# Kernel optimization log

Measured on AMD Instinct MI355X. Metric: run time of the kernel, lower is better.

Reference implementation:

```python
import jax, jax.numpy as jnp
import numpy as np

DIM = 2048
N_EXPERTS = 16
TOP_K = 4
MOE_INTER = 1024
SHARED_INTER = 2 * MOE_INTER  # n_shared_experts * moe_inter_dim
B, S = 4, 1024
INIT = 0.02


def setup_inputs() -> dict:
    key = jax.random.key(0)
    ks = jax.random.split(key, 8)
    return {
        "x": jax.random.normal(ks[0], (B, S, DIM), dtype=jnp.float32),
        "gate_w": jax.random.normal(ks[1], (DIM, N_EXPERTS), dtype=jnp.float32) * INIT,
        "w1": jax.random.normal(ks[2], (N_EXPERTS, DIM, MOE_INTER), dtype=jnp.float32) * INIT,
        "w2": jax.random.normal(ks[3], (N_EXPERTS, MOE_INTER, DIM), dtype=jnp.float32) * INIT,
        "w3": jax.random.normal(ks[4], (N_EXPERTS, DIM, MOE_INTER), dtype=jnp.float32) * INIT,
        "ws1": jax.random.normal(ks[5], (DIM, SHARED_INTER), dtype=jnp.float32) * INIT,
        "ws2": jax.random.normal(ks[6], (SHARED_INTER, DIM), dtype=jnp.float32) * INIT,
        "ws3": jax.random.normal(ks[7], (DIM, SHARED_INTER), dtype=jnp.float32) * INIT,
    }


def _moe_forward(x, gate_w, w1, w2, w3, ws1, ws2, ws3):
    shape = x.shape
    xf = x.reshape(-1, DIM)  # [T, D]
    # Gate: softmax scores, top-k selection (weights are the top-k probs)
    scores = jax.nn.softmax(xf @ gate_w, axis=-1)          # [T, E]
    weights, indices = jax.lax.top_k(scores, TOP_K)         # [T, K] each
    y = jnp.zeros_like(xf)
    # Fixed loop over experts (structural, not over data dims).
    for e in range(N_EXPERTS):
        # gate coefficient for expert e: 0 if not in token's top-k
        coef = jnp.sum(weights * (indices == e), axis=-1)   # [T]
        h = jax.nn.silu(xf @ w1[e]) * (xf @ w3[e])          # [T, I]
        y = y + coef[:, None] * (h @ w2[e])
    # Shared experts (always-on gated MLP)
    z = (jax.nn.silu(xf @ ws1) * (xf @ ws3)) @ ws2
    return (y + z).reshape(shape)


def reference(x, gate_w, w1, w2, w3, ws1, ws2, ws3):
    return _moe_forward(x, gate_w, w1, w2, w3, ws1, ws2, ws3)
```

## Files before the change

kernel.cpp:

```cpp
#include <hip/hip_runtime.h>
#include <hip/hip_bf16.h>
#include <stdint.h>

#define T_TOK 4096
#define DIMD  2048
#define NEXP  16
#define TOPK  4
#define NI    1024
#define NSH   2048

typedef __attribute__((ext_vector_type(8))) short short8;
typedef __attribute__((ext_vector_type(4))) float f32x4;
typedef __attribute__((ext_vector_type(4))) unsigned short u16x4;

__device__ __forceinline__ unsigned short f2bf(float f) {
    union { float f; unsigned u; } v; v.f = f;
    return (unsigned short)((v.u + 0x7fffu + ((v.u >> 16) & 1u)) >> 16);
}

__device__ __forceinline__ void gload16(const void* g, void* l) {
    __builtin_amdgcn_global_load_lds(
        (const __attribute__((address_space(1))) void*)g,
        (__attribute__((address_space(3))) void*)l, 16, 0, 0);
}

__global__ __launch_bounds__(256) void gwt_kernel(const float* __restrict__ gw,
                                                  float* __restrict__ gwT) {
    int i = blockIdx.x * 256 + threadIdx.x;
    int d = i >> 4, e = i & 15;
    gwT[e * DIMD + d] = gw[i];
}

__global__ __launch_bounds__(256) void gate_kernel(const float* __restrict__ x,
                                                   const float* __restrict__ gwT,
                                                   int* __restrict__ blk_cnt,
                                                   int* __restrict__ tk_er,
                                                   float* __restrict__ tk_wv) {
    __shared__ int h[16];
    const int blk = blockIdx.x;
    const int t = blk * 4 + (threadIdx.x >> 6);
    const int lane = threadIdx.x & 63;
    if (threadIdx.x < 16) h[threadIdx.x] = 0;
    __syncthreads();

    const f32x4* xr = (const f32x4*)(x + (size_t)t * DIMD);
    f32x4 xv[8];
#pragma unroll
    for (int i = 0; i < 8; ++i) xv[i] = xr[i * 64 + lane];

    float acc[NEXP];
#pragma unroll
    for (int e = 0; e < NEXP; ++e) {
        const f32x4* gr = (const f32x4*)(gwT + e * DIMD);
        float s = 0.f;
#pragma unroll
        for (int i = 0; i < 8; ++i) {
            f32x4 gv = gr[i * 64 + lane];
            s += xv[i][0] * gv[0] + xv[i][1] * gv[1] +
                 xv[i][2] * gv[2] + xv[i][3] * gv[3];
        }
        acc[e] = s;
    }
#pragma unroll
    for (int e = 0; e < NEXP; ++e) {
        float v = acc[e];
#pragma unroll
        for (int off = 32; off; off >>= 1) v += __shfl_xor(v, off, 64);
        acc[e] = v;
    }
    float m = acc[0];
#pragma unroll
    for (int e = 1; e < NEXP; ++e) m = fmaxf(m, acc[e]);
    float s = 0.f;
#pragma unroll
    for (int e = 0; e < NEXP; ++e) { acc[e] = expf(acc[e] - m); s += acc[e]; }
    float inv = 1.f / s;
#pragma unroll
    for (int e = 0; e < NEXP; ++e) acc[e] *= inv;

    float w4[TOPK]; int i4[TOPK];
#pragma unroll
    for (int k = 0; k < TOPK; ++k) {
        float bv = -1.f; int be = 0;
#pragma unroll
        for (int e = 0; e < NEXP; ++e)
            if (acc[e] > bv) { bv = acc[e]; be = e; }
        w4[k] = bv; i4[k] = be;
#pragma unroll
        for (int e = 0; e < NEXP; ++e)
            if (e == be) acc[e] = -1.f;
    }

    if (lane == 0) {
        int r4[TOPK];
#pragma unroll
        for (int k = 0; k < TOPK; ++k) r4[k] = atomicAdd(&h[i4[k]], 1);
#pragma unroll
        for (int k = 0; k < TOPK; ++k) {
            tk_er[t * 4 + k] = (i4[k] << 20) | r4[k];
            tk_wv[t * 4 + k] = w4[k];
        }
    }
    __syncthreads();
    if (threadIdx.x < 16) blk_cnt[blk * 16 + threadIdx.x] = h[threadIdx.x];
}

__global__ __launch_bounds__(256) void scan_kernel(const int* __restrict__ blk_cnt,
                                                   int* __restrict__ blk_off,
                                                   int* __restrict__ cnt,
                                                   int* __restrict__ offs,
                                                   int* __restrict__ table) {
    __shared__ int gsum[16][17];
    __shared__ int gbase[16][17];
    __shared__ int csh[16];
    int tid = threadIdx.x;
    int e = tid >> 4, g = tid & 15;
    {
        int s = 0;
        for (int b = g * 64; b < g * 64 + 64; ++b) s += blk_cnt[b * 16 + e];
        gsum[e][g] = s;
    }
    __syncthreads();
    if (tid < 16) {
        int run = 0;
        for (int g2 = 0; g2 < 16; ++g2) { gbase[tid][g2] = run; run += gsum[tid][g2]; }
        csh[tid] = run;
        cnt[tid] = run;
    }
    __syncthreads();
    {
        int run = gbase[e][g];
        for (int b = g * 64; b < g * 64 + 64; ++b) {
            blk_off[b * 16 + e] = run;
            run += blk_cnt[b * 16 + e];
        }
    }
    if (tid == 0) {
        int o = 0;
        for (int e2 = 0; e2 < 16; ++e2) { offs[e2] = o; o += csh[e2]; }
        offs[NEXP] = o;
        int ns = 0;
        for (int e2 = 0; e2 < 16; ++e2)
            for (int rb = 0; rb < csh[e2]; rb += 256) {
                table[ns] = e2; table[128 + ns] = rb; ++ns;
            }
        table[255] = ns;
    }
}

__global__ __launch_bounds__(256) void fill_kernel(const int* __restrict__ tk_er,
                                                   const float* __restrict__ tk_wv,
                                                   const int* __restrict__ blk_off,
                                                   int* __restrict__ list,
                                                   float* __restrict__ cw) {
    int i = blockIdx.x * 256 + threadIdx.x;
    int rec = tk_er[i];
    int e = rec >> 20, r = rec & 0xFFFFF;
    int t = i >> 2;
    int ro = blk_off[(t >> 2) * 16 + e] + r;
    list[e * T_TOK + ro] = t;
    cw[e * T_TOK + ro] = tk_wv[i];
}

__global__ __launch_bounds__(256) void cvt_kernel(const float* __restrict__ x,
                                                  unsigned short* __restrict__ xb) {
    int i = blockIdx.x * 256 + threadIdx.x;
    const f32x4* src = (const f32x4*)x;
    f32x4 a = src[i * 2 + 0];
    f32x4 b = src[i * 2 + 1];
    short8 o;
#pragma unroll
    for (int j = 0; j < 4; ++j) o[j] = (short)f2bf(a[j]);
#pragma unroll
    for (int j = 0; j < 4; ++j) o[4 + j] = (short)f2bf(b[j]);
    ((short8*)xb)[i] = o;
}

template <int MODE>
__global__ __launch_bounds__(256) void tq_kernel(const float* __restrict__ src,
                                                 unsigned short* __restrict__ dst,
                                                 int K, int N, size_t dstStrideE) {
    int e = blockIdx.z;
    src += (size_t)e * K * N;
    dst += (size_t)e * dstStrideE;
    __shared__ unsigned short tile[32][36];
    int t = threadIdx.x;
    int k0 = blockIdx.y * 32, n0 = blockIdx.x * 32;
    {
        int row = t >> 3, c4 = (t & 7) * 4;
        f32x4 v = *(const f32x4*)(src + (size_t)(k0 + row) * N + n0 + c4);
#pragma unroll
        for (int j = 0; j < 4; ++j) tile[row][c4 + j] = f2bf(v[j]);
    }
    __syncthreads();
    {
        int nn = t >> 3, kc = (t & 7) * 4;
        int n = n0 + nn;
        int r = (MODE == 0) ? n : ((n >> 4) * 32 + (MODE == 2 ? 16 : 0) + (n & 15));
        u16x4 o;
#pragma unroll
        for (int j = 0; j < 4; ++j) o[j] = tile[kc + j][nn];
        *(u16x4*)(dst + (size_t)r * K + k0 + kc) = o;
    }
}


#define STA4(base, kt) do { \
    gload16(gA[0][0] + (kt) * 64, (void*)(smem + (base) + ldsA[0][0])); \
    gload16(gA[0][1] + (kt) * 64, (void*)(smem + (base) + ldsA[0][1])); \
    gload16(gA[1][0] + (kt) * 64, (void*)(smem + (base) + ldsA[1][0])); \
    gload16(gA[1][1] + (kt) * 64, (void*)(smem + (base) + ldsA[1][1])); \
  } while (0)
#define STBU(base, kt, u) do { \
    gload16(gB[u][0] + (kt) * 64, (void*)(smem + (base) + ldsB[u][0])); \
    gload16(gB[u][1] + (kt) * 64, (void*)(smem + (base) + ldsB[u][1])); \
  } while (0)

#define RDA(base, MH) do { \
    _Pragma("unroll") \
    for (int m2 = 0; m2 < 4; ++m2) { \
      const char* bp = smem + (base) + (wm * 128 + (MH) * 64 + m2 * 16 + fr) * 128; \
      aF[m2][0] = *(const short8*)(bp + kA0); \
      aF[m2][1] = *(const short8*)(bp + kA1); \
    } } while (0)
#define RDB(dst, base, NH) do { \
    _Pragma("unroll") \
    for (int n2 = 0; n2 < 2; ++n2) { \
      const char* bp = smem + (base) + (wn * 64 + (NH) * 32 + n2 * 16 + fr) * 128; \
      dst[n2][0] = *(const short8*)(bp + kA0); \
      dst[n2][1] = *(const short8*)(bp + kA1); \
    } } while (0)

#define MM(MH, NH, BF) do { \
    __builtin_amdgcn_s_setprio(1); \
    _Pragma("unroll") \
    for (int m2 = 0; m2 < 4; ++m2) { \
      _Pragma("unroll") \
      for (int n2 = 0; n2 < 2; ++n2) { \
        acc[(MH) * 4 + m2][(NH) * 2 + n2] = __builtin_amdgcn_mfma_f32_16x16x32_bf16( \
            aF[m2][0], BF[n2][0], acc[(MH) * 4 + m2][(NH) * 2 + n2], 0, 0, 0); \
        acc[(MH) * 4 + m2][(NH) * 2 + n2] = __builtin_amdgcn_mfma_f32_16x16x32_bf16( \
            aF[m2][1], BF[n2][1], acc[(MH) * 4 + m2][(NH) * 2 + n2], 0, 0, 0); \
      } \
    } \
    __builtin_amdgcn_s_setprio(0); \
  } while (0)

template <int KIND>
__global__ __launch_bounds__(512, 2) void gemm8p(
    const unsigned short* __restrict__ A, const unsigned short* __restrict__ Ball,
    const int* __restrict__ cnt, const int* __restrict__ offs,
    const int* __restrict__ list, const float* __restrict__ cw,
    unsigned short* __restrict__ hout, float* __restrict__ fout,
    const int* __restrict__ table) {
    constexpr bool ROUTED = (KIND == 1 || KIND == 3);
    constexpr bool UP = (KIND <= 1);
    constexpr int K = (KIND <= 1) ? 2048 : 1024;
    constexpr int NT = K / 64;
    constexpr int ASTR = (KIND == 3) ? 1024 : 2048;
    constexpr int BSTR = (KIND == 3) ? 1024 : 2048;

    int bx, rb, e, M, obase;
    if constexpr (ROUTED) {
        int bid = blockIdx.x;
        int slot = bid >> 3;
        if (slot >= table[255]) return;
        bx = bid & 7;
        e = table[slot];
        rb = table[128 + slot];
        M = cnt[e];
        obase = offs[e];
    } else {
        bx = blockIdx.x; rb = blockIdx.y * 256; e = 0; M = T_TOK; obase = 0;
    }
    const int kb = (KIND == 2) ? blockIdx.z * 1024 : 0;
    const unsigned short* Bp = Ball +
        (KIND == 1 ? (size_t)e * 2048 * 2048 : KIND == 3 ? (size_t)e * 2048 * 1024 : 0);

    extern __shared__ char smem[];

    const int tid = threadIdx.x;
    const int lane = tid & 63, wid = tid >> 6;
    const int wm = wid >> 2, wn = wid & 3;
    const int fr = lane & 15, fq = lane >> 4;
    const int swz = (fr & 7) << 4;
    const int kA0 = (fq * 16) ^ swz;
    const int kA1 = (64 + fq * 16) ^ swz;

    int ldsA[2][2], ldsB[2][2];
    const unsigned short* gA[2][2];
    const unsigned short* gB[2][2];
#pragma unroll
    for (int u = 0; u < 2; ++u)
#pragma unroll
        for (int i = 0; i < 2; ++i) {
            int rowA = i * 128 + u * 64 + (tid >> 3);
            int kcA = (tid & 7) ^ (rowA & 7);
            ldsA[u][i] = i * 16384 + u * 8192 + tid * 16;
            int gr = rb + rowA;
            int cr = (gr < M) ? gr : (M - 1);
            size_t arow;
            if (KIND == 1)      arow = (size_t)list[e * T_TOK + cr];
            else if (KIND == 3) arow = (size_t)(obase + cr);
            else                arow = (size_t)gr;
            gA[u][i] = A + arow * ASTR + kb + kcA * 8;

            int s = (tid >> 8) + 2 * i;
            int rowB = s * 64 + u * 32 + ((tid >> 3) & 31);
            int kcB = (tid & 7) ^ (rowB & 7);
            ldsB[u][i] = s * 8192 + u * 4096 + (tid & 255) * 16;
            gB[u][i] = Bp + (size_t)(bx * 256 + rowB) * BSTR + kb + kcB * 8;
        }

    f32x4 acc[8][4];
#pragma unroll
    for (int m = 0; m < 8; ++m)
#pragma unroll
        for (int n = 0; n < 4; ++n) acc[m][n] = (f32x4)0.f;

    short8 aF[4][2], bF0[2][2], bF1[2][2];

    STBU(65536, 0, 0); STBU(65536, 0, 1);
    STBU(65536 + 32768, 1, 0); STBU(65536 + 32768, 1, 1);
    STA4(0, 0);
    asm volatile("s_waitcnt vmcnt(0)" ::: "memory");
    __builtin_amdgcn_s_barrier();

    int bB = 0, bB2 = 2;
    for (int t = 0; t < NT; ++t) {
        const int baseA = (t & 1) * 32768;
        const int baseAn = ((t + 1) & 1) * 32768;
        const int baseB = 65536 + bB * 32768;
        const int baseBn = 65536 + bB2 * 32768;
        const bool moreA = (t + 1 < NT);
        const bool moreB = (t + 2 < NT);

        RDA(baseA, 0); RDB(bF0, baseB, 0);
        if (moreA) STA4(baseAn, t + 1);
        if (moreB) { STBU(baseBn, t + 2, 0); STBU(baseBn, t + 2, 1); }
        MM(0, 0, bF0);
        RDB(bF1, baseB, 1);
        MM(0, 1, bF1);
        RDA(baseA, 1);
        MM(1, 1, bF1);
        MM(1, 0, bF0);
        if (moreB) { asm volatile("s_waitcnt vmcnt(4)" ::: "memory"); }
        else       { asm volatile("s_waitcnt vmcnt(0)" ::: "memory"); }
        __builtin_amdgcn_s_barrier();
        bB = (bB == 2) ? 0 : bB + 1;
        bB2 = (bB2 == 2) ? 0 : bB2 + 1;
    }

    if constexpr (UP) {
        constexpr int LDO = (KIND == 1) ? NI : NSH;
#pragma unroll
        for (int mf = 0; mf < 8; ++mf)
#pragma unroll
            for (int q = 0; q < 4; ++q) {
                int gr = rb + wm * 128 + mf * 16 + fq * 4 + q;
                if (gr < M) {
                    float coef = 1.f;
                    if constexpr (KIND == 1) coef = cw[e * T_TOK + gr];
                    size_t orow = (size_t)(obase + gr) * LDO;
#pragma unroll
                    for (int nfp = 0; nfp < 2; ++nfp) {
                        float c1 = acc[mf][2 * nfp][q], c3 = acc[mf][2 * nfp + 1][q];
                        float h = c1 / (1.f + __expf(-c1)) * c3 * coef;
                        int ncol = (bx * 8 + wn * 2 + nfp) * 16 + fr;
                        hout[orow + ncol] = f2bf(h);
                    }
                }
            }
    } else {
#pragma unroll
        for (int mf = 0; mf < 8; ++mf)
#pragma unroll
            for (int q = 0; q < 4; ++q) {
                int gr = rb + wm * 128 + mf * 16 + fq * 4 + q;
                if (gr < M) {
                    int orow = (KIND == 3) ? list[e * T_TOK + gr] : gr;
#pragma unroll
                    for (int nf = 0; nf < 4; ++nf) {
                        int col = bx * 256 + wn * 64 + nf * 16 + fr;
                        atomicAdd(fout + (size_t)orow * DIMD + col, acc[mf][nf][q]);
                    }
                }
            }
    }
}

extern "C" void kernel_launch(void* const* d_in, const int* in_sizes, int n_in,
                              void* d_out, int out_size, void* d_ws, size_t ws_size,
                              hipStream_t stream) {
    const float* x   = (const float*)d_in[0];
    const float* gw  = (const float*)d_in[1];
    const float* w1  = (const float*)d_in[2];
    const float* w2  = (const float*)d_in[3];
    const float* w3  = (const float*)d_in[4];
    const float* ws1 = (const float*)d_in[5];
    const float* ws2 = (const float*)d_in[6];
    const float* ws3 = (const float*)d_in[7];
    float* out = (float*)d_out;

    char* p = (char*)d_ws;
    unsigned short* xb   = (unsigned short*)p; p += (size_t)T_TOK * DIMD * 2;
    unsigned short* hs   = (unsigned short*)p; p += (size_t)T_TOK * NSH * 2;
    unsigned short* hbuf = (unsigned short*)p; p += (size_t)T_TOK * TOPK * NI * 2;
    unsigned short* upT  = (unsigned short*)p; p += (size_t)NEXP * 2048 * DIMD * 2;
    unsigned short* w2T  = (unsigned short*)p; p += (size_t)NEXP * DIMD * NI * 2;
    unsigned short* upsT = (unsigned short*)p; p += (size_t)2 * NSH * DIMD * 2;
    unsigned short* ws2T = (unsigned short*)p; p += (size_t)DIMD * NSH * 2;
    float* gwT = (float*)p;                    p += (size_t)NEXP * DIMD * 4;
    float* cw = (float*)p;                     p += (size_t)NEXP * T_TOK * 4;
    int* list = (int*)p;                       p += (size_t)NEXP * T_TOK * 4;
    int* tk_er = (int*)p;                      p += (size_t)T_TOK * TOPK * 4;
    float* tk_wv = (float*)p;                  p += (size_t)T_TOK * TOPK * 4;
    int* blk_cnt = (int*)p;                    p += (size_t)1024 * 16 * 4;
    int* blk_off = (int*)p;                    p += (size_t)1024 * 16 * 4;
    int* cnt = (int*)p;                        p += 256;
    int* offs = (int*)p;                       p += 256;
    int* table = (int*)p;                      p += 1024;
    if ((size_t)(p - (char*)d_ws) > ws_size) return;

    hipFuncSetAttribute((const void*)&gemm8p<0>, hipFuncAttributeMaxDynamicSharedMemorySize, 163840);
    hipFuncSetAttribute((const void*)&gemm8p<1>, hipFuncAttributeMaxDynamicSharedMemorySize, 163840);
    hipFuncSetAttribute((const void*)&gemm8p<2>, hipFuncAttributeMaxDynamicSharedMemorySize, 163840);
    hipFuncSetAttribute((const void*)&gemm8p<3>, hipFuncAttributeMaxDynamicSharedMemorySize, 163840);

    hipMemsetAsync(out, 0, (size_t)out_size * 4, stream);
    gwt_kernel<<<(NEXP * DIMD) / 256, 256, 0, stream>>>(gw, gwT);
    gate_kernel<<<T_TOK / 4, 256, 0, stream>>>(x, gwT, blk_cnt, tk_er, tk_wv);
    scan_kernel<<<1, 256, 0, stream>>>(blk_cnt, blk_off, cnt, offs, table);
    fill_kernel<<<T_TOK * TOPK / 256, 256, 0, stream>>>(tk_er, tk_wv, blk_off, list, cw);
    cvt_kernel<<<(T_TOK * DIMD / 8) / 256, 256, 0, stream>>>(x, xb);

    tq_kernel<1><<<dim3(NI / 32, DIMD / 32, NEXP), 256, 0, stream>>>(w1, upT, DIMD, NI, (size_t)2048 * DIMD);
    tq_kernel<2><<<dim3(NI / 32, DIMD / 32, NEXP), 256, 0, stream>>>(w3, upT, DIMD, NI, (size_t)2048 * DIMD);
    tq_kernel<1><<<dim3(NSH / 32, DIMD / 32, 1), 256, 0, stream>>>(ws1, upsT, DIMD, NSH, 0);
    tq_kernel<2><<<dim3(NSH / 32, DIMD / 32, 1), 256, 0, stream>>>(ws3, upsT, DIMD, NSH, 0);
    tq_kernel<0><<<dim3(DIMD / 32, NI / 32, NEXP), 256, 0, stream>>>(w2, w2T, NI, DIMD, (size_t)DIMD * NI);
    tq_kernel<0><<<dim3(DIMD / 32, NSH / 32, 1), 256, 0, stream>>>(ws2, ws2T, NSH, DIMD, 0);

    gemm8p<0><<<dim3(16, 16, 1), 512, 163840, stream>>>(
        xb, upsT, nullptr, nullptr, nullptr, nullptr, hs, nullptr, nullptr);
    gemm8p<2><<<dim3(8, 16, 2), 512, 163840, stream>>>(
        hs, ws2T, nullptr, nullptr, nullptr, nullptr, nullptr, out, nullptr);
    gemm8p<1><<<640, 512, 163840, stream>>>(
        xb, upT, cnt, offs, list, cw, hbuf, nullptr, table);
    gemm8p<3><<<640, 512, 163840, stream>>>(
        hbuf, w2T, cnt, offs, list, nullptr, nullptr, out, table);
}
```

Measured before the change: 715.4 us.

## Shrink GEMM tiles to 128x256 with BK=32 triple-buffered pipeline for higher occupancy

Reworks the bf16 MFMA GEMM from 256x256 tiles with BK=64 and a large LDS footprint to 128x256 tiles with BK=32 and a 3-stage ring buffer in 72KB of LDS. Launch bounds rise to 4 blocks per CU, the grids and the routed slot table double (the table now packs expert and row base into one int), and a new swizzled LDS read layout is added. The aim is more concurrent waves and less padding waste on the routed experts. The cost is lower reuse per tile, more global loads per FLOP, and more atomic and barrier overhead.

```diff
diff --git a/kernel.cpp b/kernel.cpp
--- a/kernel.cpp
+++ b/kernel.cpp
@@ -141,8 +141,8 @@
         offs[NEXP] = o;
         int ns = 0;
         for (int e2 = 0; e2 < 16; ++e2)
-            for (int rb = 0; rb < csh[e2]; rb += 256) {
-                table[ns] = e2; table[128 + ns] = rb; ++ns;
+            for (int rb = 0; rb < csh[e2]; rb += 128) {
+                table[ns] = (e2 << 16) | rb; ++ns;
             }
         table[255] = ns;
     }
@@ -204,50 +204,8 @@
     }
 }
 
-
-#define STA4(base, kt) do { \
-    gload16(gA[0][0] + (kt) * 64, (void*)(smem + (base) + ldsA[0][0])); \
-    gload16(gA[0][1] + (kt) * 64, (void*)(smem + (base) + ldsA[0][1])); \
-    gload16(gA[1][0] + (kt) * 64, (void*)(smem + (base) + ldsA[1][0])); \
-    gload16(gA[1][1] + (kt) * 64, (void*)(smem + (base) + ldsA[1][1])); \
-  } while (0)
-#define STBU(base, kt, u) do { \
-    gload16(gB[u][0] + (kt) * 64, (void*)(smem + (base) + ldsB[u][0])); \
-    gload16(gB[u][1] + (kt) * 64, (void*)(smem + (base) + ldsB[u][1])); \
-  } while (0)
-
-#define RDA(base, MH) do { \
-    _Pragma("unroll") \
-    for (int m2 = 0; m2 < 4; ++m2) { \
-      const char* bp = smem + (base) + (wm * 128 + (MH) * 64 + m2 * 16 + fr) * 128; \
-      aF[m2][0] = *(const short8*)(bp + kA0); \
-      aF[m2][1] = *(const short8*)(bp + kA1); \
-    } } while (0)
-#define RDB(dst, base, NH) do { \
-    _Pragma("unroll") \
-    for (int n2 = 0; n2 < 2; ++n2) { \
-      const char* bp = smem + (base) + (wn * 64 + (NH) * 32 + n2 * 16 + fr) * 128; \
-      dst[n2][0] = *(const short8*)(bp + kA0); \
-      dst[n2][1] = *(const short8*)(bp + kA1); \
-    } } while (0)
-
-#define MM(MH, NH, BF) do { \
-    __builtin_amdgcn_s_setprio(1); \
-    _Pragma("unroll") \
-    for (int m2 = 0; m2 < 4; ++m2) { \
-      _Pragma("unroll") \
-      for (int n2 = 0; n2 < 2; ++n2) { \
-        acc[(MH) * 4 + m2][(NH) * 2 + n2] = __builtin_amdgcn_mfma_f32_16x16x32_bf16( \
-            aF[m2][0], BF[n2][0], acc[(MH) * 4 + m2][(NH) * 2 + n2], 0, 0, 0); \
-        acc[(MH) * 4 + m2][(NH) * 2 + n2] = __builtin_amdgcn_mfma_f32_16x16x32_bf16( \
-            aF[m2][1], BF[n2][1], acc[(MH) * 4 + m2][(NH) * 2 + n2], 0, 0, 0); \
-      } \
-    } \
-    __builtin_amdgcn_s_setprio(0); \
-  } while (0)
-
 template <int KIND>
-__global__ __launch_bounds__(512, 2) void gemm8p(
+__global__ __launch_bounds__(512, 4) void gemm8p(
     const unsigned short* __restrict__ A, const unsigned short* __restrict__ Ball,
     const int* __restrict__ cnt, const int* __restrict__ offs,
     const int* __restrict__ list, const float* __restrict__ cw,
@@ -256,7 +214,7 @@
     constexpr bool ROUTED = (KIND == 1 || KIND == 3);
     constexpr bool UP = (KIND <= 1);
     constexpr int K = (KIND <= 1) ? 2048 : 1024;
-    constexpr int NT = K / 64;
+    constexpr int NT = K / 32;
     constexpr int ASTR = (KIND == 3) ? 1024 : 2048;
     constexpr int BSTR = (KIND == 3) ? 1024 : 2048;
 
@@ -266,12 +224,13 @@
         int slot = bid >> 3;
         if (slot >= table[255]) return;
         bx = bid & 7;
-        e = table[slot];
-        rb = table[128 + slot];
+        int pk = table[slot];
+        e = pk >> 16;
+        rb = pk & 0xFFFF;
         M = cnt[e];
         obase = offs[e];
     } else {
-        bx = blockIdx.x; rb = blockIdx.y * 256; e = 0; M = T_TOK; obase = 0;
+        bx = blockIdx.x; rb = blockIdx.y * 128; e = 0; M = T_TOK; obase = 0;
     }
     const int kb = (KIND == 2) ? blockIdx.z * 1024 : 0;
     const unsigned short* Bp = Ball +
@@ -283,88 +242,94 @@
     const int lane = tid & 63, wid = tid >> 6;
     const int wm = wid >> 2, wn = wid & 3;
     const int fr = lane & 15, fq = lane >> 4;
-    const int swz = (fr & 7) << 4;
-    const int kA0 = (fq * 16) ^ swz;
-    const int kA1 = (64 + fq * 16) ^ swz;
-
-    int ldsA[2][2], ldsB[2][2];
-    const unsigned short* gA[2][2];
-    const unsigned short* gB[2][2];
-#pragma unroll
-    for (int u = 0; u < 2; ++u)
-#pragma unroll
-        for (int i = 0; i < 2; ++i) {
-            int rowA = i * 128 + u * 64 + (tid >> 3);
-            int kcA = (tid & 7) ^ (rowA & 7);
-            ldsA[u][i] = i * 16384 + u * 8192 + tid * 16;
-            int gr = rb + rowA;
-            int cr = (gr < M) ? gr : (M - 1);
-            size_t arow;
-            if (KIND == 1)      arow = (size_t)list[e * T_TOK + cr];
-            else if (KIND == 3) arow = (size_t)(obase + cr);
-            else                arow = (size_t)gr;
-            gA[u][i] = A + arow * ASTR + kb + kcA * 8;
-
-            int s = (tid >> 8) + 2 * i;
-            int rowB = s * 64 + u * 32 + ((tid >> 3) & 31);
-            int kcB = (tid & 7) ^ (rowB & 7);
-            ldsB[u][i] = s * 8192 + u * 4096 + (tid & 255) * 16;
-            gB[u][i] = Bp + (size_t)(bx * 256 + rowB) * BSTR + kb + kcB * 8;
-        }
-
-    f32x4 acc[8][4];
-#pragma unroll
-    for (int m = 0; m < 8; ++m)
+    const int offR = ((fr >> 1) << 7) + (((((fr & 1) << 2) | fq) ^ (fr >> 1)) << 4);
+    const int d16 = tid * 16;
+
+    const unsigned short* pA;
+    const unsigned short* pB0;
+    const unsigned short* pB1;
+    {
+        int c = tid, s = c >> 3, sl = (c & 7) ^ (s & 7);
+        int rA = 2 * s + (sl >> 2), kk = (sl & 3) * 8;
+        int gr = rb + rA;
+        int cr = (gr < M) ? gr : (M - 1);
+        size_t arow;
+        if (KIND == 1)      arow = (size_t)list[e * T_TOK + cr];
+        else if (KIND == 3) arow = (size_t)(obase + cr);
+        else                arow = (size_t)gr;
+        pA = A + arow * ASTR + kb + kk;
+    }
+#pragma unroll
+    for (int u = 0; u < 2; ++u) {
+        int c = u * 512 + tid, s = c >> 3, sl = (c & 7) ^ (s & 7);
+        int rB = 2 * s + (sl >> 2), kk = (sl & 3) * 8;
+        const unsigned short* p = Bp + (size_t)(bx * 256 + rB) * BSTR + kb + kk;
+        if (u == 0) pB0 = p; else pB1 = p;
+    }
+
+    f32x4 acc[4][4];
+#pragma unroll
+    for (int m = 0; m < 4; ++m)
 #pragma unroll
         for (int n = 0; n < 4; ++n) acc[m][n] = (f32x4)0.f;
 
-    short8 aF[4][2], bF0[2][2], bF1[2][2];
-
-    STBU(65536, 0, 0); STBU(65536, 0, 1);
-    STBU(65536 + 32768, 1, 0); STBU(65536 + 32768, 1, 1);
-    STA4(0, 0);
+    gload16(pA,      (void*)(smem + 0 + d16));
+    gload16(pA + 32, (void*)(smem + 8192 + d16));
+    gload16(pB0,      (void*)(smem + 24576 + d16));
+    gload16(pB1,      (void*)(smem + 24576 + 8192 + d16));
+    gload16(pB0 + 32, (void*)(smem + 24576 + 16384 + d16));
+    gload16(pB1 + 32, (void*)(smem + 24576 + 16384 + 8192 + d16));
+    pA += 64; pB0 += 64; pB1 += 64;
     asm volatile("s_waitcnt vmcnt(0)" ::: "memory");
     __builtin_amdgcn_s_barrier();
 
-    int bB = 0, bB2 = 2;
+    int bA = 0, bA2 = 16384;
+    int bB = 0, bB2 = 32768;
     for (int t = 0; t < NT; ++t) {
-        const int baseA = (t & 1) * 32768;
-        const int baseAn = ((t + 1) & 1) * 32768;
-        const int baseB = 65536 + bB * 32768;
-        const int baseBn = 65536 + bB2 * 32768;
-        const bool moreA = (t + 1 < NT);
-        const bool moreB = (t + 2 < NT);
-
-        RDA(baseA, 0); RDB(bF0, baseB, 0);
-        if (moreA) STA4(baseAn, t + 1);
-        if (moreB) { STBU(baseBn, t + 2, 0); STBU(baseBn, t + 2, 1); }
-        MM(0, 0, bF0);
-        RDB(bF1, baseB, 1);
-        MM(0, 1, bF1);
-        RDA(baseA, 1);
-        MM(1, 1, bF1);
-        MM(1, 0, bF0);
-        if (moreB) { asm volatile("s_waitcnt vmcnt(4)" ::: "memory"); }
-        else       { asm volatile("s_waitcnt vmcnt(0)" ::: "memory"); }
+        short8 aF[4], bF[4];
+#pragma unroll
+        for (int m = 0; m < 4; ++m)
+            aF[m] = *(const short8*)(smem + bA + wm * 4096 + m * 1024 + offR);
+#pragma unroll
+        for (int n = 0; n < 4; ++n)
+            bF[n] = *(const short8*)(smem + 24576 + bB + wn * 4096 + n * 1024 + offR);
+        const bool more = (t + 2 < NT);
+        if (more) {
+            gload16(pA, (void*)(smem + bA2 + d16));
+            gload16(pB0, (void*)(smem + 24576 + bB2 + d16));
+            gload16(pB1, (void*)(smem + 24576 + bB2 + 8192 + d16));
+            pA += 32; pB0 += 32; pB1 += 32;
+        }
+        __builtin_amdgcn_s_setprio(1);
+#pragma unroll
+        for (int m = 0; m < 4; ++m)
+#pragma unroll
+            for (int n = 0; n < 4; ++n)
+                acc[m][n] = __builtin_amdgcn_mfma_f32_16x16x32_bf16(aF[m], bF[n], acc[m][n], 0, 0, 0);
+        __builtin_amdgcn_s_setprio(0);
+        if (more) { asm volatile("s_waitcnt vmcnt(3)" ::: "memory"); }
+        else      { asm volatile("s_waitcnt vmcnt(0)" ::: "memory"); }
         __builtin_amdgcn_s_barrier();
-        bB = (bB == 2) ? 0 : bB + 1;
-        bB2 = (bB2 == 2) ? 0 : bB2 + 1;
+        bA = (bA == 16384) ? 0 : bA + 8192;
+        bA2 = (bA2 == 16384) ? 0 : bA2 + 8192;
+        bB = (bB == 32768) ? 0 : bB + 16384;
+        bB2 = (bB2 == 32768) ? 0 : bB2 + 16384;
     }
 
     if constexpr (UP) {
         constexpr int LDO = (KIND == 1) ? NI : NSH;
 #pragma unroll
-        for (int mf = 0; mf < 8; ++mf)
+        for (int m = 0; m < 4; ++m)
 #pragma unroll
             for (int q = 0; q < 4; ++q) {
-                int gr = rb + wm * 128 + mf * 16 + fq * 4 + q;
+                int gr = rb + wm * 64 + m * 16 + fq * 4 + q;
                 if (gr < M) {
                     float coef = 1.f;
                     if constexpr (KIND == 1) coef = cw[e * T_TOK + gr];
                     size_t orow = (size_t)(obase + gr) * LDO;
 #pragma unroll
                     for (int nfp = 0; nfp < 2; ++nfp) {
-                        float c1 = acc[mf][2 * nfp][q], c3 = acc[mf][2 * nfp + 1][q];
+                        float c1 = acc[m][2 * nfp][q], c3 = acc[m][2 * nfp + 1][q];
                         float h = c1 / (1.f + __expf(-c1)) * c3 * coef;
                         int ncol = (bx * 8 + wn * 2 + nfp) * 16 + fr;
                         hout[orow + ncol] = f2bf(h);
@@ -373,16 +338,16 @@
             }
     } else {
 #pragma unroll
-        for (int mf = 0; mf < 8; ++mf)
+        for (int m = 0; m < 4; ++m)
 #pragma unroll
             for (int q = 0; q < 4; ++q) {
-                int gr = rb + wm * 128 + mf * 16 + fq * 4 + q;
+                int gr = rb + wm * 64 + m * 16 + fq * 4 + q;
                 if (gr < M) {
                     int orow = (KIND == 3) ? list[e * T_TOK + gr] : gr;
 #pragma unroll
                     for (int nf = 0; nf < 4; ++nf) {
                         int col = bx * 256 + wn * 64 + nf * 16 + fr;
-                        atomicAdd(fout + (size_t)orow * DIMD + col, acc[mf][nf][q]);
+                        atomicAdd(fout + (size_t)orow * DIMD + col, acc[m][nf][q]);
                     }
                 }
             }
@@ -422,10 +387,10 @@
     int* table = (int*)p;                      p += 1024;
     if ((size_t)(p - (char*)d_ws) > ws_size) return;
 
-    hipFuncSetAttribute((const void*)&gemm8p<0>, hipFuncAttributeMaxDynamicSharedMemorySize, 163840);
-    hipFuncSetAttribute((const void*)&gemm8p<1>, hipFuncAttributeMaxDynamicSharedMemorySize, 163840);
-    hipFuncSetAttribute((const void*)&gemm8p<2>, hipFuncAttributeMaxDynamicSharedMemorySize, 163840);
-    hipFuncSetAttribute((const void*)&gemm8p<3>, hipFuncAttributeMaxDynamicSharedMemorySize, 163840);
+    hipFuncSetAttribute((const void*)&gemm8p<0>, hipFuncAttributeMaxDynamicSharedMemorySize, 73728);
+    hipFuncSetAttribute((const void*)&gemm8p<1>, hipFuncAttributeMaxDynamicSharedMemorySize, 73728);
+    hipFuncSetAttribute((const void*)&gemm8p<2>, hipFuncAttributeMaxDynamicSharedMemorySize, 73728);
+    hipFuncSetAttribute((const void*)&gemm8p<3>, hipFuncAttributeMaxDynamicSharedMemorySize, 73728);
 
     hipMemsetAsync(out, 0, (size_t)out_size * 4, stream);
     gwt_kernel<<<(NEXP * DIMD) / 256, 256, 0, stream>>>(gw, gwT);
@@ -441,12 +406,12 @@
     tq_kernel<0><<<dim3(DIMD / 32, NI / 32, NEXP), 256, 0, stream>>>(w2, w2T, NI, DIMD, (size_t)DIMD * NI);
     tq_kernel<0><<<dim3(DIMD / 32, NSH / 32, 1), 256, 0, stream>>>(ws2, ws2T, NSH, DIMD, 0);
 
-    gemm8p<0><<<dim3(16, 16, 1), 512, 163840, stream>>>(
+    gemm8p<0><<<dim3(16, 32, 1), 512, 73728, stream>>>(
         xb, upsT, nullptr, nullptr, nullptr, nullptr, hs, nullptr, nullptr);
-    gemm8p<2><<<dim3(8, 16, 2), 512, 163840, stream>>>(
+    gemm8p<2><<<dim3(8, 32, 2), 512, 73728, stream>>>(
         hs, ws2T, nullptr, nullptr, nullptr, nullptr, nullptr, out, nullptr);
-    gemm8p<1><<<640, 512, 163840, stream>>>(
+    gemm8p<1><<<1152, 512, 73728, stream>>>(
         xb, upT, cnt, offs, list, cw, hbuf, nullptr, table);
-    gemm8p<3><<<640, 512, 163840, stream>>>(
+    gemm8p<3><<<1152, 512, 73728, stream>>>(
         hbuf, w2T, cnt, offs, list, nullptr, nullptr, out, table);
 }
```

Measured after the change: 708.0 us. About the same (-1.0%).
